# Performance work log

Hardware: AMD Instinct MI355X
Metric: run time of the kernel (lower is better)

Reference implementation:

```python
import jax, jax.numpy as jnp
import numpy as np

DIM = 256
NUM_HEADS = 4
HEAD_DIM = DIM // NUM_HEADS
SCALE = HEAD_DIM ** -0.5


def setup_inputs() -> dict:
    key = jax.random.key(0)
    ks = jax.random.split(key, 9)
    B, P, C = 4, 4096, DIM
    s = 0.02
    return {
        "x": jax.random.normal(ks[0], (B, P, C), dtype=jnp.float32),
        "Wq": jax.random.normal(ks[1], (C, C), dtype=jnp.float32) * s,
        "bq": jnp.zeros((C,), dtype=jnp.float32),
        "Wk": jax.random.normal(ks[2], (C, C), dtype=jnp.float32) * s,
        "bk": jnp.zeros((C,), dtype=jnp.float32),
        "Wv": jax.random.normal(ks[3], (C, C), dtype=jnp.float32) * s,
        "bv": jnp.zeros((C,), dtype=jnp.float32),
        "Wo": jax.random.normal(ks[4], (C, C), dtype=jnp.float32) * s,
        "bo": jnp.zeros((C,), dtype=jnp.float32),
    }


def reference(x, Wq, bq, Wk, bk, Wv, bv, Wo, bo):
    B, P, C = x.shape
    H, D = NUM_HEADS, C // NUM_HEADS
    q = (x @ Wq + bq).reshape(B, P, H, D)
    k = (x @ Wk + bk).reshape(B, P, H, D)
    v = (x @ Wv + bv).reshape(B, P, H, D)
    # att[b,p,q,h] = sum_d q[b,p,h,d]*scale * k[b,q,h,d]
    att = jnp.einsum('bphd,bqhd->bpqh', q * SCALE, k)
    att = jax.nn.softmax(att, axis=2)
    out = jnp.einsum('bpqh,bqhd->bphd', att, v).reshape(B, P, C)
    return out @ Wo + bo
```

## Files before the change

kernel.cpp:

```cpp
#include <hip/hip_runtime.h>
#include <hip/hip_bf16.h>

#define DIMC 256
#define NHEADS 4
#define HDIM 64
#define BATCH 4
#define SEQ 4096
#define MTOT (BATCH*SEQ)
#define SCALE_LOG2E 0.18033688011112042f

typedef __attribute__((ext_vector_type(8))) __bf16 bf16x8;
typedef __attribute__((ext_vector_type(4))) __bf16 bf16x4;
typedef __attribute__((ext_vector_type(2))) __bf16 bf16x2;
typedef __attribute__((ext_vector_type(4))) float f32x4;
typedef __attribute__((ext_vector_type(2))) unsigned uint2v;
typedef __attribute__((ext_vector_type(4))) unsigned uint4v;

__device__ inline void gll16(const void* g, void* l) {
  __builtin_amdgcn_global_load_lds((const __attribute__((address_space(1))) unsigned int*)g,
                                   (__attribute__((address_space(3))) unsigned int*)l, 16, 0, 0);
}

__device__ inline float vexp2(float x) { return __builtin_amdgcn_exp2f(x); }

__device__ inline unsigned pack2(float lo, float hi) {
  bf16x2 p; p[0] = (__bf16)lo; p[1] = (__bf16)hi;
  return __builtin_bit_cast(unsigned, p);
}

__device__ inline bf16x8 swzread(const __bf16* base, int row, int c16) {
  return *reinterpret_cast<const bf16x8*>(
      reinterpret_cast<const char*>(base) + row * 128 + ((c16 ^ (row & 7)) << 4));
}


__global__ __launch_bounds__(256) void cvt_x_kernel(const float* __restrict__ x, __bf16* __restrict__ xb) {
  int i = (blockIdx.x * 256 + threadIdx.x) * 4;
  float4 v = *reinterpret_cast<const float4*>(x + i);
  bf16x4 o;
  o[0] = (__bf16)v.x; o[1] = (__bf16)v.y; o[2] = (__bf16)v.z; o[3] = (__bf16)v.w;
  *reinterpret_cast<bf16x4*>(xb + i) = o;
}

__global__ __launch_bounds__(256) void prep_w(const float* __restrict__ Wq, const float* __restrict__ Wk,
                                              const float* __restrict__ Wv, const float* __restrict__ Wo,
                                              const float* __restrict__ bq, const float* __restrict__ bk,
                                              const float* __restrict__ bv,
                                              __bf16* __restrict__ wqkvt, __bf16* __restrict__ wot,
                                              float* __restrict__ biasq) {
  int row = blockIdx.x;
  int k = threadIdx.x;
  if (row < 768) {
    const float* src; float scale = 1.f; int n = row & 255;
    if (row < 256)      { src = Wq; scale = SCALE_LOG2E; }
    else if (row < 512) { src = Wk; }
    else                { src = Wv; }
    wqkvt[row * 256 + k] = (__bf16)(src[k * 256 + n] * scale);
  } else if (row < 1024) {
    int n = row - 768;
    wot[n * 256 + k] = (__bf16)(Wo[k * 256 + n]);
  } else {
    int i = (row - 1024) * 256 + k;
    biasq[i] = (i < 256) ? bq[i] * SCALE_LOG2E : (i < 512 ? bk[i - 256] : bv[i - 512]);
  }
}

template<int MODE>
__global__ __launch_bounds__(256) void gemm_bt(const __bf16* __restrict__ A, const __bf16* __restrict__ Bt,
                                               const float* __restrict__ bias,
                                               __bf16* __restrict__ q_ws, __bf16* __restrict__ k_ws,
                                               __bf16* __restrict__ vt_ws, float* __restrict__ fout) {
  __shared__ __align__(16) __bf16 As[128 * 64];
  __shared__ __align__(16) __bf16 Bs[128 * 64];
  const int tid = threadIdx.x;
  const int lane = tid & 63, wave = tid >> 6;
  const int wr = wave >> 1, wc = wave & 1;
  const int r16 = lane & 15, g4 = lane >> 4;
  const int m0 = blockIdx.y * 128, n0 = blockIdx.x * 128;
  f32x4 acc[4][4] = {};
  for (int k0 = 0; k0 < DIMC; k0 += 64) {
    #pragma unroll
    for (int it = 0; it < 4; ++it) {
      int e = it * 256 + tid;
      int r = e >> 3, c = e & 7;
      int cs = c ^ (r & 7);
      gll16(A  + (size_t)(m0 + r) * DIMC + k0 + cs * 8, As + e * 8);
      gll16(Bt + (size_t)(n0 + r) * DIMC + k0 + cs * 8, Bs + e * 8);
    }
    __syncthreads();
    #pragma unroll
    for (int kk = 0; kk < 2; ++kk) {
      bf16x8 af[4], bfr[4];
      #pragma unroll
      for (int mi = 0; mi < 4; ++mi)
        af[mi] = swzread(As, wr * 64 + mi * 16 + r16, kk * 4 + g4);
      #pragma unroll
      for (int ni = 0; ni < 4; ++ni)
        bfr[ni] = swzread(Bs, wc * 64 + ni * 16 + r16, kk * 4 + g4);
      #pragma unroll
      for (int mi = 0; mi < 4; ++mi)
        #pragma unroll
        for (int ni = 0; ni < 4; ++ni)
          acc[mi][ni] = __builtin_amdgcn_mfma_f32_16x16x32_bf16(af[mi], bfr[ni], acc[mi][ni], 0, 0, 0);
    }
    __syncthreads();
  }
  #pragma unroll
  for (int mi = 0; mi < 4; ++mi)
    #pragma unroll
    for (int ni = 0; ni < 4; ++ni)
      #pragma unroll
      for (int r = 0; r < 4; ++r) {
        int m = m0 + wr * 64 + mi * 16 + g4 * 4 + r;
        int n = n0 + wc * 64 + ni * 16 + r16;
        float v = acc[mi][ni][r] + bias[n];
        if (MODE == 0) {
          int b = m >> 12, p = m & 4095;
          int sect = n >> 8, nc = n & 255;
          int h = nc >> 6, d = nc & 63;
          __bf16 hv = (__bf16)v;
          size_t bhb = (size_t)(b * NHEADS + h);
          if (sect == 0)      q_ws[(bhb * SEQ + p) * HDIM + d] = hv;
          else if (sect == 1) k_ws[(bhb * SEQ + p) * HDIM + d] = hv;
          else                vt_ws[(bhb * HDIM + d) * SEQ + p] = hv;
        } else {
          fout[(size_t)m * DIMC + n] = v;
        }
      }
}

__global__ __launch_bounds__(256, 4) void attn_kernel(const __bf16* __restrict__ q_ws, const __bf16* __restrict__ k_ws,
                                                      const __bf16* __restrict__ vt_ws,
                                                      float* __restrict__ o_num, float* __restrict__ lsum) {
  __shared__ __align__(16) __bf16 Ks[2][64 * 64];
  __shared__ __align__(16) __bf16 Vts[2][64 * 64];
  const int tid = threadIdx.x;
  const int lane = tid & 63;
  const int r16 = lane & 15, g4 = lane >> 4;
  int bid = blockIdx.x;
  int wg = (bid & 7) * 128 + (bid >> 3);
  int bh = wg >> 6, rrw = wg & 63;
  int qb = rrw >> 1, half = rrw & 1;
  int b = bh >> 2, h = bh & 3;
  const __bf16* Qp  = q_ws  + (size_t)bh * SEQ * HDIM;
  const __bf16* Kp  = k_ws  + (size_t)bh * SEQ * HDIM;
  const __bf16* Vtp = vt_ws + (size_t)bh * HDIM * SEQ;
  const int q0 = qb * 128 + (tid >> 6) * 32;
  const int kvb = half * (SEQ / 2);
  bf16x8 qf[2][2];
  #pragma unroll
  for (int hh = 0; hh < 2; ++hh)
    #pragma unroll
    for (int kk = 0; kk < 2; ++kk)
      qf[hh][kk] = *reinterpret_cast<const bf16x8*>(Qp + (size_t)(q0 + hh * 16 + r16) * HDIM + kk * 32 + g4 * 8);
  f32x4 o_acc[2][4] = {};
  f32x4 rsv[2] = {};

  const int sr = tid >> 3;
  const int scs = (tid & 7) ^ (sr & 7);
  const __bf16* kSrc = Kp  + (size_t)sr * HDIM + scs * 8;
  const __bf16* vSrc = Vtp + (size_t)sr * SEQ  + scs * 8;

  #define STAGE(buf, kv0) do { \
      gll16(kSrc + (size_t)(kv0) * HDIM,        &Ks[buf][tid * 8]); \
      gll16(kSrc + (size_t)((kv0) + 32) * HDIM, &Ks[buf][(tid + 256) * 8]); \
      gll16(vSrc + (kv0),                       &Vts[buf][tid * 8]); \
      gll16(vSrc + 32 * SEQ + (kv0),            &Vts[buf][(tid + 256) * 8]); \
    } while (0)

  STAGE(0, kvb);
  __syncthreads();

  int cur = 0;
  for (int t = 0; t < SEQ / 128; ++t) {
    if (t + 1 < SEQ / 128) STAGE(cur ^ 1, kvb + (t + 1) * 64);
    f32x4 s0[4] = {}, s1[4] = {};
    __builtin_amdgcn_s_setprio(1);
    #pragma unroll
    for (int ni = 0; ni < 4; ++ni)
      #pragma unroll
      for (int kk = 0; kk < 2; ++kk) {
        bf16x8 kf = swzread(Ks[cur], ni * 16 + r16, kk * 4 + g4);
        s0[ni] = __builtin_amdgcn_mfma_f32_16x16x32_bf16(kf, qf[0][kk], s0[ni], 0, 0, 0);
        s1[ni] = __builtin_amdgcn_mfma_f32_16x16x32_bf16(kf, qf[1][kk], s1[ni], 0, 0, 0);
      }
    __builtin_amdgcn_s_setprio(0);
    bf16x8 pa[2][2];
    #pragma unroll
    for (int hh = 0; hh < 2; ++hh) {
      unsigned c[4][2];
      #pragma unroll
      for (int ni = 0; ni < 4; ++ni) {
        const f32x4& sv = hh ? s1[ni] : s0[ni];
        float p0 = vexp2(sv[0]), p1 = vexp2(sv[1]);
        float p2 = vexp2(sv[2]), p3 = vexp2(sv[3]);
        rsv[hh] += (f32x4){p0, p1, p2, p3};
        c[ni][0] = pack2(p0, p1);
        c[ni][1] = pack2(p2, p3);
      }
      unsigned tt[2][4];
      #pragma unroll
      for (int kk = 0; kk < 2; ++kk)
        #pragma unroll
        for (int u = 0; u < 2; ++u) {
          uint2v p = __builtin_amdgcn_permlane32_swap(c[2 * kk][u], c[2 * kk + 1][u], false, false);
          uint2v q = __builtin_amdgcn_permlane16_swap(p[0], p[1], false, false);
          tt[kk][u]     = q[0];
          tt[kk][2 + u] = q[1];
        }
      uint4v w0 = {tt[0][0], tt[0][1], tt[0][2], tt[0][3]};
      uint4v w1 = {tt[1][0], tt[1][1], tt[1][2], tt[1][3]};
      pa[hh][0] = __builtin_bit_cast(bf16x8, w0);
      pa[hh][1] = __builtin_bit_cast(bf16x8, w1);
    }
    __builtin_amdgcn_s_setprio(1);
    #pragma unroll
    for (int kk = 0; kk < 2; ++kk)
      #pragma unroll
      for (int di = 0; di < 4; ++di) {
        bf16x8 vf = swzread(Vts[cur], di * 16 + r16, kk * 4 + g4);
        o_acc[0][di] = __builtin_amdgcn_mfma_f32_16x16x32_bf16(pa[0][kk], vf, o_acc[0][di], 0, 0, 0);
        o_acc[1][di] = __builtin_amdgcn_mfma_f32_16x16x32_bf16(pa[1][kk], vf, o_acc[1][di], 0, 0, 0);
      }
    __builtin_amdgcn_s_setprio(0);
    __syncthreads();
    cur ^= 1;
  }
  #pragma unroll
  for (int hh = 0; hh < 2; ++hh) {
    float den = (rsv[hh][0] + rsv[hh][1]) + (rsv[hh][2] + rsv[hh][3]);
    den += __shfl_xor(den, 16);
    den += __shfl_xor(den, 32);
    if (lane < 16) atomicAdd(&lsum[(size_t)bh * SEQ + q0 + hh * 16 + r16], den);
  }
  #pragma unroll
  for (int hh = 0; hh < 2; ++hh)
    #pragma unroll
    for (int di = 0; di < 4; ++di)
      #pragma unroll
      for (int r = 0; r < 4; ++r) {
        int q = q0 + hh * 16 + g4 * 4 + r;
        atomicAdd(&o_num[(size_t)(b * SEQ + q) * DIMC + h * HDIM + di * 16 + r16], o_acc[hh][di][r]);
      }
}

__global__ __launch_bounds__(256) void normalize_o(const float* __restrict__ on, const float* __restrict__ lsum,
                                                   __bf16* __restrict__ o_ws) {
  int i = blockIdx.x * 256 + threadIdx.x;
  int flat = i * 4;
  int m = flat >> 8, c = flat & 255;
  int h = c >> 6;
  int b = m >> 12, p = m & 4095;
  float inv = 1.f / lsum[(size_t)(b * NHEADS + h) * SEQ + p];
  float4 n = *reinterpret_cast<const float4*>(on + flat);
  bf16x4 o;
  o[0] = (__bf16)(n.x * inv); o[1] = (__bf16)(n.y * inv);
  o[2] = (__bf16)(n.z * inv); o[3] = (__bf16)(n.w * inv);
  *reinterpret_cast<bf16x4*>(o_ws + flat) = o;
}


extern "C" void kernel_launch(void* const* d_in, const int* in_sizes, int n_in,
                              void* d_out, int out_size, void* d_ws, size_t ws_size,
                              hipStream_t stream) {
  const float* x  = (const float*)d_in[0];
  const float* Wq = (const float*)d_in[1];
  const float* bq = (const float*)d_in[2];
  const float* Wk = (const float*)d_in[3];
  const float* bk = (const float*)d_in[4];
  const float* Wv = (const float*)d_in[5];
  const float* bv = (const float*)d_in[6];
  const float* Wo = (const float*)d_in[7];
  const float* bo = (const float*)d_in[8];
  float* out = (float*)d_out;

  const size_t NE = (size_t)MTOT * DIMC;
  char* w = (char*)d_ws;
  __bf16* q_ws  = (__bf16*)w; w += NE * 2;
  __bf16* k_ws  = (__bf16*)w; w += NE * 2;
  __bf16* vt_ws = (__bf16*)w; w += NE * 2;
  __bf16* wqkvt = (__bf16*)w; w += (size_t)768 * 256 * 2;
  __bf16* wot   = (__bf16*)w; w += (size_t)256 * 256 * 2;
  float*  biasq = (float*)w;  w += 768 * 4;
  float*  lsum  = (float*)w;  w += (size_t)16 * SEQ * 4;
  float*  o_num = (float*)w;  w += NE * 4;
  __bf16* xb   = (__bf16*)o_num;
  __bf16* o_ws = q_ws;

  cvt_x_kernel<<<MTOT * DIMC / 1024, 256, 0, stream>>>(x, xb);
  prep_w<<<1027, 256, 0, stream>>>(Wq, Wk, Wv, Wo, bq, bk, bv, wqkvt, wot, biasq);
  gemm_bt<0><<<dim3(6, 128), 256, 0, stream>>>(xb, wqkvt, biasq, q_ws, k_ws, vt_ws, nullptr);
  hipMemsetAsync(lsum, 0, (size_t)16 * SEQ * 4 + NE * 4, stream);
  attn_kernel<<<1024, 256, 0, stream>>>(q_ws, k_ws, vt_ws, o_num, lsum);
  normalize_o<<<NE / 1024, 256, 0, stream>>>(o_num, lsum, o_ws);
  gemm_bt<1><<<dim3(2, 128), 256, 0, stream>>>(o_ws, wot, bo, nullptr, nullptr, nullptr, out);
}
```

Measured before the change: 138.3 us.

## Switch attention kernel MFMAs from 16x16x32 to 32x32x16 bf16 tiles

Rewrites the attention inner loop to use 32x32x16 bf16 MFMA instructions instead of 16x16x32. Each wave now covers 32 query rows with one accumulator per 32-column block. The P-matrix repacking needs only permlane32 swaps, and the row-sum reduction becomes a single scalar per lane. The aim is fewer MFMA issues, fewer LDS fragment reads and a cheaper softmax relayout, at the cost of larger per-instruction latency and different register pressure.

```diff
diff --git a/kernel.cpp b/kernel.cpp
--- a/kernel.cpp
+++ b/kernel.cpp
@@ -13,6 +13,7 @@
 typedef __attribute__((ext_vector_type(4))) __bf16 bf16x4;
 typedef __attribute__((ext_vector_type(2))) __bf16 bf16x2;
 typedef __attribute__((ext_vector_type(4))) float f32x4;
+typedef __attribute__((ext_vector_type(16))) float f32x16;
 typedef __attribute__((ext_vector_type(2))) unsigned uint2v;
 typedef __attribute__((ext_vector_type(4))) unsigned uint4v;
 
@@ -136,7 +137,7 @@
   __shared__ __align__(16) __bf16 Vts[2][64 * 64];
   const int tid = threadIdx.x;
   const int lane = tid & 63;
-  const int r16 = lane & 15, g4 = lane >> 4;
+  const int l31 = lane & 31, h5 = lane >> 5;
   int bid = blockIdx.x;
   int wg = (bid & 7) * 128 + (bid >> 3);
   int bh = wg >> 6, rrw = wg & 63;
@@ -147,14 +148,12 @@
   const __bf16* Vtp = vt_ws + (size_t)bh * HDIM * SEQ;
   const int q0 = qb * 128 + (tid >> 6) * 32;
   const int kvb = half * (SEQ / 2);
-  bf16x8 qf[2][2];
+  bf16x8 qf[4];
   #pragma unroll
-  for (int hh = 0; hh < 2; ++hh)
-    #pragma unroll
-    for (int kk = 0; kk < 2; ++kk)
-      qf[hh][kk] = *reinterpret_cast<const bf16x8*>(Qp + (size_t)(q0 + hh * 16 + r16) * HDIM + kk * 32 + g4 * 8);
-  f32x4 o_acc[2][4] = {};
-  f32x4 rsv[2] = {};
+  for (int ks = 0; ks < 4; ++ks)
+    qf[ks] = *reinterpret_cast<const bf16x8*>(Qp + (size_t)(q0 + l31) * HDIM + ks * 16 + h5 * 8);
+  f32x16 o_acc[2] = {};
+  float den = 0.f;
 
   const int sr = tid >> 3;
   const int scs = (tid & 7) ^ (sr & 7);
@@ -174,74 +173,59 @@
   int cur = 0;
   for (int t = 0; t < SEQ / 128; ++t) {
     if (t + 1 < SEQ / 128) STAGE(cur ^ 1, kvb + (t + 1) * 64);
-    f32x4 s0[4] = {}, s1[4] = {};
+    f32x16 s[2] = {};
     __builtin_amdgcn_s_setprio(1);
     #pragma unroll
-    for (int ni = 0; ni < 4; ++ni)
-      #pragma unroll
-      for (int kk = 0; kk < 2; ++kk) {
-        bf16x8 kf = swzread(Ks[cur], ni * 16 + r16, kk * 4 + g4);
-        s0[ni] = __builtin_amdgcn_mfma_f32_16x16x32_bf16(kf, qf[0][kk], s0[ni], 0, 0, 0);
-        s1[ni] = __builtin_amdgcn_mfma_f32_16x16x32_bf16(kf, qf[1][kk], s1[ni], 0, 0, 0);
+    for (int ni = 0; ni < 2; ++ni)
+      #pragma unroll
+      for (int ks = 0; ks < 4; ++ks) {
+        bf16x8 kf = swzread(Ks[cur], ni * 32 + l31, ks * 2 + h5);
+        s[ni] = __builtin_amdgcn_mfma_f32_32x32x16_bf16(kf, qf[ks], s[ni], 0, 0, 0);
       }
     __builtin_amdgcn_s_setprio(0);
-    bf16x8 pa[2][2];
-    #pragma unroll
-    for (int hh = 0; hh < 2; ++hh) {
-      unsigned c[4][2];
-      #pragma unroll
-      for (int ni = 0; ni < 4; ++ni) {
-        const f32x4& sv = hh ? s1[ni] : s0[ni];
-        float p0 = vexp2(sv[0]), p1 = vexp2(sv[1]);
-        float p2 = vexp2(sv[2]), p3 = vexp2(sv[3]);
-        rsv[hh] += (f32x4){p0, p1, p2, p3};
-        c[ni][0] = pack2(p0, p1);
-        c[ni][1] = pack2(p2, p3);
-      }
-      unsigned tt[2][4];
-      #pragma unroll
-      for (int kk = 0; kk < 2; ++kk)
-        #pragma unroll
-        for (int u = 0; u < 2; ++u) {
-          uint2v p = __builtin_amdgcn_permlane32_swap(c[2 * kk][u], c[2 * kk + 1][u], false, false);
-          uint2v q = __builtin_amdgcn_permlane16_swap(p[0], p[1], false, false);
-          tt[kk][u]     = q[0];
-          tt[kk][2 + u] = q[1];
-        }
-      uint4v w0 = {tt[0][0], tt[0][1], tt[0][2], tt[0][3]};
-      uint4v w1 = {tt[1][0], tt[1][1], tt[1][2], tt[1][3]};
-      pa[hh][0] = __builtin_bit_cast(bf16x8, w0);
-      pa[hh][1] = __builtin_bit_cast(bf16x8, w1);
+    float E[2][16];
+    #pragma unroll
+    for (int ni = 0; ni < 2; ++ni)
+      #pragma unroll
+      for (int r = 0; r < 16; ++r) {
+        float e = vexp2(s[ni][r]);
+        E[ni][r] = e;
+        den += e;
+      }
+    bf16x8 pa[4];
+    #pragma unroll
+    for (int ks = 0; ks < 4; ++ks) {
+      const int ni = ks >> 1, base = (ks & 1) * 8;
+      unsigned A0 = pack2(E[ni][base + 0], E[ni][base + 1]);
+      unsigned A1 = pack2(E[ni][base + 2], E[ni][base + 3]);
+      unsigned B0 = pack2(E[ni][base + 4], E[ni][base + 5]);
+      unsigned B1 = pack2(E[ni][base + 6], E[ni][base + 7]);
+      uint2v r0 = __builtin_amdgcn_permlane32_swap(A0, B0, false, false);
+      uint2v r1 = __builtin_amdgcn_permlane32_swap(A1, B1, false, false);
+      uint4v w = {r0[0], r1[0], r0[1], r1[1]};
+      pa[ks] = __builtin_bit_cast(bf16x8, w);
     }
     __builtin_amdgcn_s_setprio(1);
     #pragma unroll
-    for (int kk = 0; kk < 2; ++kk)
-      #pragma unroll
-      for (int di = 0; di < 4; ++di) {
-        bf16x8 vf = swzread(Vts[cur], di * 16 + r16, kk * 4 + g4);
-        o_acc[0][di] = __builtin_amdgcn_mfma_f32_16x16x32_bf16(pa[0][kk], vf, o_acc[0][di], 0, 0, 0);
-        o_acc[1][di] = __builtin_amdgcn_mfma_f32_16x16x32_bf16(pa[1][kk], vf, o_acc[1][di], 0, 0, 0);
+    for (int ks = 0; ks < 4; ++ks)
+      #pragma unroll
+      for (int di = 0; di < 2; ++di) {
+        bf16x8 vf = swzread(Vts[cur], di * 32 + l31, ks * 2 + h5);
+        o_acc[di] = __builtin_amdgcn_mfma_f32_32x32x16_bf16(pa[ks], vf, o_acc[di], 0, 0, 0);
       }
     __builtin_amdgcn_s_setprio(0);
     __syncthreads();
     cur ^= 1;
   }
+  den += __shfl_xor(den, 32);
+  if (lane < 32) atomicAdd(&lsum[(size_t)bh * SEQ + q0 + l31], den);
   #pragma unroll
-  for (int hh = 0; hh < 2; ++hh) {
-    float den = (rsv[hh][0] + rsv[hh][1]) + (rsv[hh][2] + rsv[hh][3]);
-    den += __shfl_xor(den, 16);
-    den += __shfl_xor(den, 32);
-    if (lane < 16) atomicAdd(&lsum[(size_t)bh * SEQ + q0 + hh * 16 + r16], den);
-  }
-  #pragma unroll
-  for (int hh = 0; hh < 2; ++hh)
-    #pragma unroll
-    for (int di = 0; di < 4; ++di)
-      #pragma unroll
-      for (int r = 0; r < 4; ++r) {
-        int q = q0 + hh * 16 + g4 * 4 + r;
-        atomicAdd(&o_num[(size_t)(b * SEQ + q) * DIMC + h * HDIM + di * 16 + r16], o_acc[hh][di][r]);
-      }
+  for (int di = 0; di < 2; ++di)
+    #pragma unroll
+    for (int r = 0; r < 16; ++r) {
+      int q = q0 + (r & 3) + 8 * (r >> 2) + 4 * h5;
+      atomicAdd(&o_num[(size_t)(b * SEQ + q) * DIMC + h * HDIM + di * 32 + l31], o_acc[di][r]);
+    }
 }
 
 __global__ __launch_bounds__(256) void normalize_o(const float* __restrict__ on, const float* __restrict__ lsum,
```

Result: slower. 141.4 us (+2.2%).
